# Performance work log

Hardware: AMD Instinct MI355X
Metric: run time of the kernel (lower is better)

Reference implementation:

```python
import jax, jax.numpy as jnp
import numpy as np

B, N, K = 2, 8192, 16
C_IN, C_OUT = 32, 64
EPS = 1e-6


def _bn(x, g, b, axes):
    m = jnp.mean(x, axes, keepdims=True)
    v = jnp.var(x, axes, keepdims=True)
    return (x - m) * jax.lax.rsqrt(v + EPS) * g + b


def _leaky(x, s):
    return jnp.where(x >= 0, x, s * x)


def _knn(coords, k):
    # brute-force euclidean KNN, self point included (dist 0)
    sq = jnp.sum(coords * coords, -1)  # (B,N)
    d2 = sq[:, :, None] + sq[:, None, :] - 2.0 * jnp.einsum('bnd,bmd->bnm', coords, coords)
    neg, idx = jax.lax.top_k(-d2, k)  # (B,N,K)
    dist = jnp.sqrt(jnp.clip(-neg, 1e-12, None))
    return idx, dist


def setup_inputs() -> dict:
    key = jax.random.key(0)
    ks = jax.random.split(key, 12)
    h = C_OUT // 2
    w = lambda k, s: jax.random.normal(k, s, jnp.float32) * 0.05
    return {
        'coords': jax.random.normal(ks[0], (B, N, 3), jnp.float32),
        'features': jax.random.normal(ks[1], (B, N, C_IN), jnp.float32),
        'W_mlp1': w(ks[2], (C_IN, h)), 'b_mlp1': jnp.zeros(h, jnp.float32),
        'W_lse1': w(ks[3], (10, h)), 'b_lse1': jnp.zeros(h, jnp.float32),
        'g_lse1': jnp.ones(h, jnp.float32), 'be_lse1': jnp.zeros(h, jnp.float32),
        'W_att1_lin': w(ks[4], (C_OUT, C_OUT)),
        'W_att1_mlp': w(ks[5], (C_OUT, h)), 'b_att1_mlp': jnp.zeros(h, jnp.float32),
        'g_att1': jnp.ones(h, jnp.float32), 'be_att1': jnp.zeros(h, jnp.float32),
        'W_lse2': w(ks[6], (10, h)), 'b_lse2': jnp.zeros(h, jnp.float32),
        'g_lse2': jnp.ones(h, jnp.float32), 'be_lse2': jnp.zeros(h, jnp.float32),
        'W_att2_lin': w(ks[7], (C_OUT, C_OUT)),
        'W_att2_mlp': w(ks[8], (C_OUT, C_OUT)), 'b_att2_mlp': jnp.zeros(C_OUT, jnp.float32),
        'g_att2': jnp.ones(C_OUT, jnp.float32), 'be_att2': jnp.zeros(C_OUT, jnp.float32),
        'W_mlp2': w(ks[9], (C_OUT, 2 * C_OUT)), 'b_mlp2': jnp.zeros(2 * C_OUT, jnp.float32),
        'W_short': w(ks[10], (C_IN, 2 * C_OUT)), 'b_short': jnp.zeros(2 * C_OUT, jnp.float32),
        'g_short': jnp.ones(2 * C_OUT, jnp.float32), 'be_short': jnp.zeros(2 * C_OUT, jnp.float32),
    }


def _forward(coords, features, W_mlp1, b_mlp1, W_lse1, b_lse1, g_lse1, be_lse1,
             W_att1_lin, W_att1_mlp, b_att1_mlp, g_att1, be_att1,
             W_lse2, b_lse2, g_lse2, be_lse2,
             W_att2_lin, W_att2_mlp, b_att2_mlp, g_att2, be_att2,
             W_mlp2, b_mlp2, W_short, b_short, g_short, be_short):
    idx, dist = _knn(coords, K)                     # (B,N,K)
    nbr = jax.vmap(lambda c, i: c[i])(coords, idx)  # gather neighbor coords (B,N,K,3)
    center = jnp.broadcast_to(coords[:, :, None, :], nbr.shape)
    # spatial encoding: [center, neighbor, center-neighbor, dist] -> 10 channels
    se = jnp.concatenate([center, nbr, center - nbr, dist[..., None]], -1)  # (B,N,K,10)

    # mlp1 (1x1 conv + LeakyReLU(0.2)), no BN
    x = _leaky(features @ W_mlp1 + b_mlp1, 0.2)     # (B,N,h)

    # LocSE 1: shared MLP (BN train-mode + ReLU) on spatial enc, concat features
    sp1 = jax.nn.relu(_bn(se @ W_lse1 + b_lse1, g_lse1, be_lse1, (0, 1, 2)))  # (B,N,K,h)
    x1 = jnp.concatenate([sp1, jnp.broadcast_to(x[:, :, None, :], sp1.shape)], -1)  # (B,N,K,2h)

    # attention pooling 1: softmax over neighbors K, weighted sum, MLP+BN+ReLU
    sc1 = jax.nn.softmax(x1 @ W_att1_lin, axis=2)
    p1 = jnp.sum(sc1 * x1, axis=2)                  # (B,N,2h)
    x = jax.nn.relu(_bn(p1 @ W_att1_mlp + b_att1_mlp, g_att1, be_att1, (0, 1)))  # (B,N,h)

    # LocSE 2 + attention pooling 2 (same KNN, separate weights)
    sp2 = jax.nn.relu(_bn(se @ W_lse2 + b_lse2, g_lse2, be_lse2, (0, 1, 2)))
    x2 = jnp.concatenate([sp2, jnp.broadcast_to(x[:, :, None, :], sp2.shape)], -1)
    sc2 = jax.nn.softmax(x2 @ W_att2_lin, axis=2)
    p2 = jnp.sum(sc2 * x2, axis=2)
    x = jax.nn.relu(_bn(p2 @ W_att2_mlp + b_att2_mlp, g_att2, be_att2, (0, 1)))  # (B,N,C_OUT)

    # mlp2 (no BN, no act) + shortcut (BN, no act), residual LeakyReLU(0.01)
    x = x @ W_mlp2 + b_mlp2                          # (B,N,2*C_OUT)
    short = _bn(features @ W_short + b_short, g_short, be_short, (0, 1))
    out = _leaky(x + short, 0.01)
    # match torch layout (B, 2*C_OUT, N, 1)
    return jnp.transpose(out, (0, 2, 1))[..., None]


def reference(coords, features, W_mlp1, b_mlp1, W_lse1, b_lse1, g_lse1, be_lse1,
              W_att1_lin, W_att1_mlp, b_att1_mlp, g_att1, be_att1,
              W_lse2, b_lse2, g_lse2, be_lse2,
              W_att2_lin, W_att2_mlp, b_att2_mlp, g_att2, be_att2,
              W_mlp2, b_mlp2, W_short, b_short, g_short, be_short):
    return _forward(coords, features, W_mlp1, b_mlp1, W_lse1, b_lse1, g_lse1, be_lse1,
                    W_att1_lin, W_att1_mlp, b_att1_mlp, g_att1, be_att1,
                    W_lse2, b_lse2, g_lse2, be_lse2,
                    W_att2_lin, W_att2_mlp, b_att2_mlp, g_att2, be_att2,
                    W_mlp2, b_mlp2, W_short, b_short, g_short, be_short)
```

## Files before the change

kernel.cpp:

```cpp
#include <hip/hip_runtime.h>
#include <cfloat>
#include <cmath>

#define DEV __device__ __forceinline__

constexpr int BB = 2, NN = 8192, KK = 16, CIN = 32, HH = 32, CO = 64, C2 = 128;
constexpr int BNTOT = BB * NN;
constexpr int BNKROWS = BB * NN * KK;
constexpr float EPSF = 1e-6f;

constexpr int S_LSE1 = 0, S_LSE2 = 64, S_ATT1 = 128, S_ATT2 = 192, S_SHORT = 320, S_TOTAL = 576;

constexpr size_t OFF_CP4   = 0;
constexpr size_t OFF_SE    = OFF_CP4 + (size_t)BNTOT * 4;
constexpr size_t OFF_XF    = OFF_SE + (size_t)BNKROWS * 10;
constexpr size_t OFF_SHORT = OFF_XF + (size_t)BNTOT * HH;
constexpr size_t OFF_PRE1  = OFF_SHORT + (size_t)BNTOT * C2;
constexpr size_t OFF_PRE2  = OFF_PRE1 + (size_t)BNTOT * HH;
constexpr size_t OFF_STATS = OFF_PRE2 + (size_t)BNTOT * CO;

__global__ __launch_bounds__(256) void k_prep(const float* __restrict__ coords,
                                              float4* __restrict__ cp4) {
#pragma clang fp contract(off)
    int i = blockIdx.x * 256 + threadIdx.x;
    if (i >= BNTOT) return;
    float x = coords[3 * i], y = coords[3 * i + 1], z = coords[3 * i + 2];
    float sq = (x * x + y * y) + z * z;
    cp4[i] = make_float4(x, y, z, sq);
}

DEV float dist2(float4 qc, float4 c) {
#pragma clang fp contract(off)
    float dot = (qc.x * c.x + qc.y * c.y) + qc.z * c.z;
    return (qc.w + c.w) - 2.0f * dot;
}

DEV unsigned encf(float f) {
    unsigned u = __float_as_uint(f);
    return (u & 0x80000000u) ? ~u : (u | 0x80000000u);
}
DEV float decf(unsigned e) {
    unsigned u = (e & 0x80000000u) ? (e & 0x7FFFFFFFu) : ~e;
    return __uint_as_float(u);
}

DEV void ins16(float (&dl)[16], int (&il)[16], float d, int id) {
    float dk = d; int jk = id;
#pragma unroll
    for (int r = 0; r < 16; ++r) {
        bool c = dk < dl[r];
        float td = dl[r]; int ti = il[r];
        dl[r] = c ? dk : dl[r]; il[r] = c ? jk : il[r];
        dk = c ? td : dk; jk = c ? ti : jk;
    }
}

DEV void ins16_lex(float (&dl)[16], int (&il)[16], float d, int id) {
    float dk = d; int jk = id;
#pragma unroll
    for (int r = 0; r < 16; ++r) {
        bool c = (dk < dl[r]) || (dk == dl[r] && jk < il[r]);
        float td = dl[r]; int ti = il[r];
        dl[r] = c ? dk : dl[r]; il[r] = c ? jk : il[r];
        dk = c ? td : dk; jk = c ? ti : jk;
    }
}

__global__ __launch_bounds__(256) void k_knn(const float4* __restrict__ cp4,
                                             float* __restrict__ se) {
    __shared__ float mdl[16][16][17];
    __shared__ int   mil[16][16][17];
    __shared__ unsigned thr[16];
    uint2 (*buf)[256] = reinterpret_cast<uint2(*)[256]>(&mdl[0][0][0]);

    int t = threadIdx.x;
    int b = blockIdx.x >> 9;
    int qbase = (blockIdx.x & 511) * 16;
    int ql = t & 15, part = t >> 4;
    const float4* cp = cp4 + (size_t)b * NN;
    float4 qc = cp[qbase + ql];

    if (t < 16) thr[t] = encf(FLT_MAX);
    __syncthreads();

    float dl[16]; int il[16];
#pragma unroll
    for (int i = 0; i < 16; ++i) { dl[i] = FLT_MAX; il[i] = 0; }

    int cb = part * 512;
#pragma unroll
    for (int k = 0; k < 16; ++k) ins16(dl, il, dist2(qc, cp[cb + k]), cb + k);
    atomicMin(&thr[ql], encf(dl[15]));
    float Tf = dl[15];
    int cnt = 0;

    float4 n0 = cp[cb + 16], n1 = cp[cb + 17], n2 = cp[cb + 18], n3 = cp[cb + 19];
    unsigned te = thr[ql];
    for (int j = cb + 16; j < cb + 512; j += 4) {
        float4 c0 = n0, c1 = n1, c2 = n2, c3 = n3;
        n0 = cp[j + 4]; n1 = cp[j + 5]; n2 = cp[j + 6]; n3 = cp[j + 7];
        float d0 = dist2(qc, c0), d1 = dist2(qc, c1), d2v = dist2(qc, c2), d3 = dist2(qc, c3);
        bool p0 = d0 <= Tf, p1 = d1 <= Tf, p2 = d2v <= Tf, p3 = d3 <= Tf;
        if (__any(p0 | p1 | p2 | p3)) {
            if (p0) { buf[cnt][t] = make_uint2(__float_as_uint(d0), (unsigned)(j)); ++cnt; }
            if (p1) { buf[cnt][t] = make_uint2(__float_as_uint(d1), (unsigned)(j + 1)); ++cnt; }
            if (p2) { buf[cnt][t] = make_uint2(__float_as_uint(d2v), (unsigned)(j + 2)); ++cnt; }
            if (p3) { buf[cnt][t] = make_uint2(__float_as_uint(d3), (unsigned)(j + 3)); ++cnt; }
            if (__any(cnt >= 4)) {
#pragma unroll
                for (int s = 0; s < 7; ++s) {
                    if (s < cnt) {
                        uint2 v = buf[s][t];
                        float d = __uint_as_float(v.x);
                        if (d < dl[15]) ins16(dl, il, d, (int)v.y);
                    }
                }
                cnt = 0;
                atomicMin(&thr[ql], encf(dl[15]));
            }
        }
        Tf = decf(te);
        te = thr[ql];
    }
    if (__any(cnt > 0)) {
#pragma unroll
        for (int s = 0; s < 7; ++s) {
            if (s < cnt) {
                uint2 v = buf[s][t];
                float d = __uint_as_float(v.x);
                if (d < dl[15]) ins16(dl, il, d, (int)v.y);
            }
        }
    }

    __syncthreads();
#pragma unroll
    for (int i = 0; i < 16; ++i) { mdl[part][ql][i] = dl[i]; mil[part][ql][i] = il[i]; }
    __syncthreads();

    for (int half = 8; half >= 1; half >>= 1) {
        if (part < half) {
#pragma unroll
            for (int i = 0; i < 16; ++i) {
                float d = mdl[part + half][ql][i]; int id = mil[part + half][ql][i];
                if (d < dl[15] || (d == dl[15] && id < il[15])) ins16_lex(dl, il, d, id);
            }
#pragma unroll
            for (int i = 0; i < 16; ++i) { mdl[part][ql][i] = dl[i]; mil[part][ql][i] = il[i]; }
        }
        __syncthreads();
    }

    {
        int qq = t >> 4, k = t & 15;
        float d2s = mdl[0][qq][k]; int id = mil[0][qq][k];
        float4 qc2 = cp[qbase + qq];
        float4 nb = cp[id];
        float dist = sqrtf(fmaxf(d2s, 1e-12f));
        float* sp = se + ((size_t)(b * NN + qbase + qq) * KK + k) * 10;
        sp[0] = qc2.x; sp[1] = qc2.y; sp[2] = qc2.z;
        sp[3] = nb.x;  sp[4] = nb.y;  sp[5] = nb.z;
        sp[6] = qc2.x - nb.x; sp[7] = qc2.y - nb.y; sp[8] = qc2.z - nb.z;
        sp[9] = dist;
    }
}

__global__ __launch_bounds__(128) void k_feat(const float* __restrict__ feat,
                                              const float* __restrict__ Wm1, const float* __restrict__ bm1,
                                              const float* __restrict__ Wsh, const float* __restrict__ bsh,
                                              float* __restrict__ xf, float* __restrict__ short_pre,
                                              double* __restrict__ stats) {
    __shared__ float fl[32][33];
    int t = threadIdx.x;
    int pbase = blockIdx.x * 32;
    float wcol[32];
#pragma unroll
    for (int i = 0; i < 32; ++i) wcol[i] = Wsh[i * C2 + t];
    float wm[32];
    if (t < 32) {
#pragma unroll
        for (int i = 0; i < 32; ++i) wm[i] = Wm1[i * HH + t];
    }
    float bs = bsh[t];
    float bm = (t < 32) ? bm1[t] : 0.f;
    double s = 0.0, s2 = 0.0;

    for (int e = t; e < 1024; e += 128) {
        int p = e >> 5, i = e & 31;
        fl[p][i] = feat[(size_t)(pbase + p) * CIN + i];
    }
    __syncthreads();
    for (int p = 0; p < 32; ++p) {
        float acc = bs;
#pragma unroll
        for (int i = 0; i < 32; ++i) acc += fl[p][i] * wcol[i];
        int gp = pbase + p;
        short_pre[(size_t)gp * C2 + t] = acc;
        s += acc; s2 += (double)acc * acc;
        if (t < 32) {
            float xv = bm;
#pragma unroll
            for (int i = 0; i < 32; ++i) xv += fl[p][i] * wm[i];
            xf[(size_t)gp * HH + t] = xv >= 0.f ? xv : 0.2f * xv;
        }
    }
    atomicAdd(&stats[S_SHORT + t], s);
    atomicAdd(&stats[S_SHORT + C2 + t], s2);
}

__global__ __launch_bounds__(256) void k_lse_stats(const float* __restrict__ se,
                                                   const float* __restrict__ W1, const float* __restrict__ b1,
                                                   const float* __restrict__ W2, const float* __restrict__ b2,
                                                   double* __restrict__ stats) {
    __shared__ float srows[256][10];
    __shared__ double red[4][64][2];
    int t = threadIdx.x;
    int c = t & 63, grp = t >> 6;
    int ch = c & 31; bool second = c >= 32;
    const float* W = second ? W2 : W1;
    float wcol[10];
#pragma unroll
    for (int d = 0; d < 10; ++d) wcol[d] = W[d * HH + ch];
    float bb = second ? b2[ch] : b1[ch];
    double s = 0.0, s2 = 0.0;
    int rbase = blockIdx.x * 512;

    for (int tile = 0; tile < 2; ++tile) {
        __syncthreads();
        const float* src = se + (size_t)(rbase + tile * 256) * 10;
        for (int e = t; e < 2560; e += 256) srows[e / 10][e % 10] = src[e];
        __syncthreads();
        int r0 = grp * 64;
        for (int r = r0; r < r0 + 64; ++r) {
            float acc = bb;
#pragma unroll
            for (int d = 0; d < 10; ++d) acc += srows[r][d] * wcol[d];
            s += acc; s2 += (double)acc * acc;
        }
    }
    red[grp][c][0] = s; red[grp][c][1] = s2;
    __syncthreads();
    if (grp == 0) {
        for (int g = 1; g < 4; ++g) { s += red[g][c][0]; s2 += red[g][c][1]; }
        int base = second ? S_LSE2 : S_LSE1;
        atomicAdd(&stats[base + ch], s);
        atomicAdd(&stats[base + 32 + ch], s2);
    }
}

DEV float2 fin_pair(const double* stats, int sbase, int ch, int nch, double M,
                    const float* g, const float* be) {
    double mean = stats[sbase + ch] / M;
    double var = stats[sbase + nch + ch] / M - mean * mean;
    double scd = (double)g[ch] / sqrt(var + (double)EPSF);
    return make_float2((float)scd, (float)((double)be[ch] - mean * scd));
}

template <int OUTC, bool SECOND>
__global__ __launch_bounds__(256) void k_att(const float* __restrict__ se,
                                             const float* __restrict__ featsrc,
                                             const float* __restrict__ Wlse, const float* __restrict__ blse,
                                             const float* __restrict__ Wlin,
                                             const float* __restrict__ Wmlp, const float* __restrict__ bmlp,
                                             double* __restrict__ stats, int lse_sbase, int feat_sbase, int stat_base,
                                             const float* __restrict__ g_lse, const float* __restrict__ be_lse,
                                             const float* __restrict__ g_f, const float* __restrict__ be_f,
                                             float* __restrict__ preout) {
    __shared__ __align__(16) float wlt[64][68];
    __shared__ float wm[64][OUTC];
    __shared__ __align__(16) float x1[4][16][40];
    __shared__ float fv[4][32];
    __shared__ float p1b[4][64];
    __shared__ double red[4][OUTC][2];

    int t = threadIdx.x, w = t >> 6, c = t & 63;
    int ch = c & 31, half = c >> 5;
    for (int e = t; e < 4096; e += 256) wlt[e & 63][e >> 6] = Wlin[e];
    for (int e = t; e < 64 * OUTC; e += 256) wm[e / OUTC][e % OUTC] = Wmlp[e];

    float wf[10]; float bf;
    {
        float2 p = fin_pair(stats, lse_sbase, ch, 32, (double)BNKROWS, g_lse, be_lse);
#pragma unroll
        for (int d = 0; d < 10; ++d) wf[d] = Wlse[d * 32 + ch] * p.x;
        bf = blse[ch] * p.x + p.y;
    }
    float fa = 1.f, fb = 0.f;
    if (SECOND && c >= 32) {
        float2 p = fin_pair(stats, feat_sbase, ch, 32, (double)BNTOT, g_f, be_f);
        fa = p.x; fb = p.y;
    }
    double s = 0.0, s2 = 0.0;
    __syncthreads();

    for (int i = 0; i < 4; ++i) {
        int p = blockIdx.x * 16 + w * 4 + i;

        int kbase = half * 8;
        const float* sp = se + (size_t)p * (KK * 10) + kbase * 10;
        float myv[8];
#pragma unroll
        for (int kk = 0; kk < 8; ++kk) {
            float acc = bf;
#pragma unroll
            for (int d = 0; d < 10; ++d) acc += sp[kk * 10 + d] * wf[d];
            myv[kk] = fmaxf(acc, 0.f);
        }
#pragma unroll
        for (int kk = 0; kk < 8; ++kk) x1[w][kbase + kk][ch] = myv[kk];

        float xv = 0.f;
        if (c >= 32) {
            xv = featsrc[(size_t)p * 32 + ch];
            if (SECOND) xv = fmaxf(xv * fa + fb, 0.f);
            fv[w][ch] = xv;
        }

        float col[16];
        if (c < 32) {
#pragma unroll
            for (int kk = 0; kk < 8; ++kk) col[kk] = myv[kk];
#pragma unroll
            for (int kk = 0; kk < 8; ++kk) col[8 + kk] = x1[w][8 + kk][ch];
        } else {
#pragma unroll
            for (int k = 0; k < 16; ++k) col[k] = xv;
        }

        float cst = 0.f;
#pragma unroll
        for (int dg = 8; dg < 16; ++dg) {
            float4 wv = *(const float4*)&wlt[c][dg * 4];
            float4 xvv = *(const float4*)&fv[w][(dg - 8) * 4];
            cst += xvv.x * wv.x + xvv.y * wv.y + xvv.z * wv.z + xvv.w * wv.w;
        }
        float scv[16];
#pragma unroll
        for (int k = 0; k < 16; ++k) scv[k] = cst;
        for (int dg = 0; dg < 8; ++dg) {
            float4 wv = *(const float4*)&wlt[c][dg * 4];
#pragma unroll
            for (int k = 0; k < 16; ++k) {
                float4 xvv = *(const float4*)&x1[w][k][dg * 4];
                scv[k] += xvv.x * wv.x + xvv.y * wv.y + xvv.z * wv.z + xvv.w * wv.w;
            }
        }
        float m = scv[0];
#pragma unroll
        for (int k = 1; k < 16; ++k) m = fmaxf(m, scv[k]);
        float sum = 0.f, p1 = 0.f;
#pragma unroll
        for (int k = 0; k < 16; ++k) { float e = __expf(scv[k] - m); sum += e; p1 += e * col[k]; }
        p1 /= sum;
        p1b[w][c] = p1;

        if (c < OUTC) {
            float acc = bmlp[c];
#pragma unroll
            for (int d = 0; d < 64; ++d) acc += p1b[w][d] * wm[d][c];
            preout[(size_t)p * OUTC + c] = acc;
            s += acc; s2 += (double)acc * acc;
        }
    }
    if (c < OUTC) { red[w][c][0] = s; red[w][c][1] = s2; }
    __syncthreads();
    if (t < OUTC) {
        double ts = red[0][t][0], ts2 = red[0][t][1];
        for (int g = 1; g < 4; ++g) { ts += red[g][t][0]; ts2 += red[g][t][1]; }
        atomicAdd(&stats[stat_base + t], ts);
        atomicAdd(&stats[stat_base + OUTC + t], ts2);
    }
}

__global__ __launch_bounds__(256) void k_out(const float* __restrict__ pre2,
                                             const float* __restrict__ short_pre,
                                             const float* __restrict__ W2, const float* __restrict__ b2,
                                             const double* __restrict__ stats,
                                             const float* __restrict__ g_a2, const float* __restrict__ be_a2,
                                             const float* __restrict__ g_s, const float* __restrict__ be_s,
                                             float* __restrict__ out) {
    __shared__ __align__(16) float w2[64][128];
    __shared__ float sc2[64], sh2[64], scs[128], shs[128], bb[128];
    int t = threadIdx.x;
    int pl = t & 31, seg = t >> 5;
    for (int e = t; e < 8192; e += 256) w2[e >> 7][e & 127] = W2[e];
    if (t < 64) { float2 p = fin_pair(stats, S_ATT2, t, 64, (double)BNTOT, g_a2, be_a2); sc2[t] = p.x; sh2[t] = p.y; }
    if (t >= 64 && t < 192) { int ch = t - 64; float2 p = fin_pair(stats, S_SHORT, ch, 128, (double)BNTOT, g_s, be_s); scs[ch] = p.x; shs[ch] = p.y; }
    if (t < 128) bb[t] = b2[t];
    __syncthreads();

    int p = blockIdx.x * 32 + pl;
    int b = p >> 13, n = p & 8191;
    const float* pr = pre2 + (size_t)p * 64;
    float xa[64];
#pragma unroll
    for (int c = 0; c < 64; c += 4) {
        float4 v = *(const float4*)&pr[c];
        xa[c + 0] = fmaxf(v.x * sc2[c + 0] + sh2[c + 0], 0.f);
        xa[c + 1] = fmaxf(v.y * sc2[c + 1] + sh2[c + 1], 0.f);
        xa[c + 2] = fmaxf(v.z * sc2[c + 2] + sh2[c + 2], 0.f);
        xa[c + 3] = fmaxf(v.w * sc2[c + 3] + sh2[c + 3], 0.f);
    }
    const float* shp = short_pre + (size_t)p * 128;
    int obase = seg * 16;
    for (int o = obase; o < obase + 16; o += 4) {
        float a0 = bb[o], a1 = bb[o + 1], a2 = bb[o + 2], a3 = bb[o + 3];
#pragma unroll
        for (int cc = 0; cc < 64; ++cc) {
            float4 wv = *(const float4*)&w2[cc][o];
            float x = xa[cc];
            a0 += x * wv.x; a1 += x * wv.y; a2 += x * wv.z; a3 += x * wv.w;
        }
        float4 sv = *(const float4*)&shp[o];
        float r0 = a0 + (sv.x * scs[o] + shs[o]);
        float r1 = a1 + (sv.y * scs[o + 1] + shs[o + 1]);
        float r2 = a2 + (sv.z * scs[o + 2] + shs[o + 2]);
        float r3 = a3 + (sv.w * scs[o + 3] + shs[o + 3]);
        out[((size_t)(b * C2 + o + 0)) * NN + n] = r0 >= 0.f ? r0 : 0.01f * r0;
        out[((size_t)(b * C2 + o + 1)) * NN + n] = r1 >= 0.f ? r1 : 0.01f * r1;
        out[((size_t)(b * C2 + o + 2)) * NN + n] = r2 >= 0.f ? r2 : 0.01f * r2;
        out[((size_t)(b * C2 + o + 3)) * NN + n] = r3 >= 0.f ? r3 : 0.01f * r3;
    }
}

extern "C" void kernel_launch(void* const* d_in, const int* in_sizes, int n_in,
                              void* d_out, int out_size, void* d_ws, size_t ws_size,
                              hipStream_t stream) {
    const float* coords    = (const float*)d_in[0];
    const float* features  = (const float*)d_in[1];
    const float* W_mlp1    = (const float*)d_in[2];
    const float* b_mlp1    = (const float*)d_in[3];
    const float* W_lse1    = (const float*)d_in[4];
    const float* b_lse1    = (const float*)d_in[5];
    const float* g_lse1    = (const float*)d_in[6];
    const float* be_lse1   = (const float*)d_in[7];
    const float* W_att1_lin= (const float*)d_in[8];
    const float* W_att1_mlp= (const float*)d_in[9];
    const float* b_att1_mlp= (const float*)d_in[10];
    const float* g_att1    = (const float*)d_in[11];
    const float* be_att1   = (const float*)d_in[12];
    const float* W_lse2    = (const float*)d_in[13];
    const float* b_lse2    = (const float*)d_in[14];
    const float* g_lse2    = (const float*)d_in[15];
    const float* be_lse2   = (const float*)d_in[16];
    const float* W_att2_lin= (const float*)d_in[17];
    const float* W_att2_mlp= (const float*)d_in[18];
    const float* b_att2_mlp= (const float*)d_in[19];
    const float* g_att2    = (const float*)d_in[20];
    const float* be_att2   = (const float*)d_in[21];
    const float* W_mlp2    = (const float*)d_in[22];
    const float* b_mlp2    = (const float*)d_in[23];
    const float* W_short   = (const float*)d_in[24];
    const float* b_short   = (const float*)d_in[25];
    const float* g_short   = (const float*)d_in[26];
    const float* be_short  = (const float*)d_in[27];

    float* ws = (float*)d_ws;
    float4* cp4      = (float4*)(ws + OFF_CP4);
    float* se        = ws + OFF_SE;
    float* xf        = ws + OFF_XF;
    float* short_pre = ws + OFF_SHORT;
    float* pre1      = ws + OFF_PRE1;
    float* pre2      = ws + OFF_PRE2;
    double* stats    = (double*)(ws + OFF_STATS);
    float* out       = (float*)d_out;

    hipMemsetAsync(stats, 0, S_TOTAL * sizeof(double), stream);

    k_prep<<<BNTOT / 256, 256, 0, stream>>>(coords, cp4);
    k_knn<<<1024, 256, 0, stream>>>(cp4, se);
    k_feat<<<512, 128, 0, stream>>>(features, W_mlp1, b_mlp1, W_short, b_short,
                                    xf, short_pre, stats);
    k_lse_stats<<<512, 256, 0, stream>>>(se, W_lse1, b_lse1, W_lse2, b_lse2, stats);
    k_att<32, false><<<1024, 256, 0, stream>>>(se, xf, W_lse1, b_lse1, W_att1_lin,
                                               W_att1_mlp, b_att1_mlp, stats,
                                               S_LSE1, 0, S_ATT1,
                                               g_lse1, be_lse1, nullptr, nullptr, pre1);
    k_att<64, true><<<1024, 256, 0, stream>>>(se, pre1, W_lse2, b_lse2, W_att2_lin,
                                              W_att2_mlp, b_att2_mlp, stats,
                                              S_LSE2, S_ATT1, S_ATT2,
                                              g_lse2, be_lse2, g_att1, be_att1, pre2);
    k_out<<<BNTOT / 32, 256, 0, stream>>>(pre2, short_pre, W_mlp2, b_mlp2, stats,
                                          g_att2, be_att2, g_short, be_short, out);
}
```

Baseline: 420.0 us.

## Seed KNN thresholds via Morton-sorted neighborhood prepass, then single-pass filtered scan

Adds a Morton-code bucketing of points (count, scan, scatter) and a seed kernel that computes an upper bound on each query's 16th-nearest distance from 256 nearby points in sorted order. The main KNN kernel then filters all candidates against this fixed bound, collects survivors into shared memory, and does a single sort per query. If a query has too many survivors it falls back to a wave-wide brute-force pass. This removes the per-thread insertion lists, atomic threshold sharing and the tree merge, at the cost of four extra small kernels and a serial per-query survivor sort.

```diff
diff --git a/kernel.cpp b/kernel.cpp
--- a/kernel.cpp
+++ b/kernel.cpp
@@ -8,6 +8,8 @@
 constexpr int BNTOT = BB * NN;
 constexpr int BNKROWS = BB * NN * KK;
 constexpr float EPSF = 1e-6f;
+constexpr int NCELL = 4096;
+constexpr int CAP = 128;
 
 constexpr int S_LSE1 = 0, S_LSE2 = 64, S_ATT1 = 128, S_ATT2 = 192, S_SHORT = 320, S_TOTAL = 576;
 
@@ -18,15 +20,68 @@
 constexpr size_t OFF_PRE1  = OFF_SHORT + (size_t)BNTOT * C2;
 constexpr size_t OFF_PRE2  = OFF_PRE1 + (size_t)BNTOT * HH;
 constexpr size_t OFF_STATS = OFF_PRE2 + (size_t)BNTOT * CO;
+constexpr size_t OFF_COUNTS= OFF_STATS + 2 * S_TOTAL;
+constexpr size_t OFF_TB    = OFF_COUNTS + 2 * NCELL;
+constexpr size_t OFF_CODE  = OFF_SHORT;
+constexpr size_t OFF_CPS   = OFF_CODE + 16384;
+constexpr size_t OFF_OIDX  = OFF_CPS + (size_t)BNTOT * 4 + 16;
+
+DEV unsigned spr3(unsigned v) {
+    return (v & 1u) | ((v & 2u) << 2) | ((v & 4u) << 4) | ((v & 8u) << 6);
+}
 
 __global__ __launch_bounds__(256) void k_prep(const float* __restrict__ coords,
-                                              float4* __restrict__ cp4) {
+                                              float4* __restrict__ cp4,
+                                              int* __restrict__ code, int* __restrict__ counts) {
 #pragma clang fp contract(off)
     int i = blockIdx.x * 256 + threadIdx.x;
     if (i >= BNTOT) return;
     float x = coords[3 * i], y = coords[3 * i + 1], z = coords[3 * i + 2];
     float sq = (x * x + y * y) + z * z;
     cp4[i] = make_float4(x, y, z, sq);
+    const float inv = 16.f / 8.8f;
+    int ix = min(15, max(0, (int)floorf((x + 4.4f) * inv)));
+    int iy = min(15, max(0, (int)floorf((y + 4.4f) * inv)));
+    int iz = min(15, max(0, (int)floorf((z + 4.4f) * inv)));
+    unsigned m = spr3(ix) | (spr3(iy) << 1) | (spr3(iz) << 2);
+    code[i] = (int)m;
+    atomicAdd(&counts[((i >> 13) << 12) + m], 1);
+}
+
+__global__ __launch_bounds__(256) void k_scan(int* __restrict__ counts) {
+    __shared__ int lds[256];
+    int t = threadIdx.x;
+    for (int b = 0; b < 2; ++b) {
+        int base = b * NCELL;
+        int v[16]; int s = 0;
+#pragma unroll
+        for (int k = 0; k < 16; ++k) { int tmp = counts[base + t * 16 + k]; v[k] = s; s += tmp; }
+        lds[t] = s;
+        __syncthreads();
+        for (int o = 1; o < 256; o <<= 1) {
+            int u = (t >= o) ? lds[t - o] : 0;
+            __syncthreads();
+            lds[t] += u;
+            __syncthreads();
+        }
+        int off = lds[t] - s;
+#pragma unroll
+        for (int k = 0; k < 16; ++k) counts[base + t * 16 + k] = off + v[k];
+        __syncthreads();
+    }
+}
+
+__global__ __launch_bounds__(256) void k_scatter(const float4* __restrict__ cp4,
+                                                 const int* __restrict__ code,
+                                                 int* __restrict__ cursor,
+                                                 float4* __restrict__ cps, int* __restrict__ oidx) {
+    int i = blockIdx.x * 256 + threadIdx.x;
+    if (i >= BNTOT) return;
+    int b = i >> 13, n = i & 8191;
+    int c = code[i];
+    int pos = atomicAdd(&cursor[(b << 12) + c], 1);
+    cps[(b << 13) + pos] = cp4[i];
+    oidx[(b << 13) + pos] = n;
 }
 
 DEV float dist2(float4 qc, float4 c) {
@@ -35,23 +90,14 @@
     return (qc.w + c.w) - 2.0f * dot;
 }
 
-DEV unsigned encf(float f) {
-    unsigned u = __float_as_uint(f);
-    return (u & 0x80000000u) ? ~u : (u | 0x80000000u);
-}
-DEV float decf(unsigned e) {
-    unsigned u = (e & 0x80000000u) ? (e & 0x7FFFFFFFu) : ~e;
-    return __uint_as_float(u);
-}
-
-DEV void ins16(float (&dl)[16], int (&il)[16], float d, int id) {
-    float dk = d; int jk = id;
+DEV void insv16(float (&dl)[16], float d) {
+    float dk = d;
 #pragma unroll
     for (int r = 0; r < 16; ++r) {
         bool c = dk < dl[r];
-        float td = dl[r]; int ti = il[r];
-        dl[r] = c ? dk : dl[r]; il[r] = c ? jk : il[r];
-        dk = c ? td : dk; jk = c ? ti : jk;
+        float td = dl[r];
+        dl[r] = c ? dk : dl[r];
+        dk = c ? td : dk;
     }
 }
 
@@ -66,94 +112,111 @@
     }
 }
 
+__global__ __launch_bounds__(256) void k_seed(const float4* __restrict__ cps,
+                                              const int* __restrict__ oidx,
+                                              float* __restrict__ tbound) {
+    int g = blockIdx.x * 256 + threadIdx.x;
+    int b = g >> 13, p = g & 8191;
+    const float4* cb_ = cps + ((size_t)b << 13);
+    float4 qc = cb_[p];
+    int s = p - 128;
+    s = s < 0 ? 0 : (s > NN - 256 ? NN - 256 : s);
+    float dl[16];
+#pragma unroll
+    for (int i = 0; i < 16; ++i) dl[i] = FLT_MAX;
+    for (int j = 0; j < 256; j += 4) {
+        float4 c0 = cb_[s + j], c1 = cb_[s + j + 1], c2 = cb_[s + j + 2], c3 = cb_[s + j + 3];
+        float d0 = dist2(qc, c0), d1 = dist2(qc, c1), d2v = dist2(qc, c2), d3 = dist2(qc, c3);
+        if (d0 < dl[15]) insv16(dl, d0);
+        if (d1 < dl[15]) insv16(dl, d1);
+        if (d2v < dl[15]) insv16(dl, d2v);
+        if (d3 < dl[15]) insv16(dl, d3);
+    }
+    tbound[(b << 13) + oidx[(b << 13) + p]] = dl[15];
+}
+
 __global__ __launch_bounds__(256) void k_knn(const float4* __restrict__ cp4,
+                                             const float* __restrict__ tbound,
                                              float* __restrict__ se) {
-    __shared__ float mdl[16][16][17];
-    __shared__ int   mil[16][16][17];
-    __shared__ unsigned thr[16];
-    uint2 (*buf)[256] = reinterpret_cast<uint2(*)[256]>(&mdl[0][0][0]);
+    __shared__ uint2 surv[16][CAP + 1];
+    __shared__ int scnt[16];
+    __shared__ float sd[16][17];
+    __shared__ int   si[16][17];
 
     int t = threadIdx.x;
     int b = blockIdx.x >> 9;
     int qbase = (blockIdx.x & 511) * 16;
     int ql = t & 15, part = t >> 4;
-    const float4* cp = cp4 + (size_t)b * NN;
-    float4 qc = cp[qbase + ql];
-
-    if (t < 16) thr[t] = encf(FLT_MAX);
-    __syncthreads();
-
-    float dl[16]; int il[16];
-#pragma unroll
-    for (int i = 0; i < 16; ++i) { dl[i] = FLT_MAX; il[i] = 0; }
+    int wv = t >> 6, lane = t & 63;
+    const float4* cp = cp4 + ((size_t)b << 13);
+    int q = qbase + ql;
+    float4 qc = cp[q];
+    float T = tbound[(b << 13) + q];
+
+    if (t < 16) scnt[t] = 0;
+    __syncthreads();
 
     int cb = part * 512;
-#pragma unroll
-    for (int k = 0; k < 16; ++k) ins16(dl, il, dist2(qc, cp[cb + k]), cb + k);
-    atomicMin(&thr[ql], encf(dl[15]));
-    float Tf = dl[15];
-    int cnt = 0;
-
-    float4 n0 = cp[cb + 16], n1 = cp[cb + 17], n2 = cp[cb + 18], n3 = cp[cb + 19];
-    unsigned te = thr[ql];
-    for (int j = cb + 16; j < cb + 512; j += 4) {
+    float4 n0 = cp[cb], n1 = cp[cb + 1], n2 = cp[cb + 2], n3 = cp[cb + 3];
+    for (int j = cb; j < cb + 512; j += 4) {
         float4 c0 = n0, c1 = n1, c2 = n2, c3 = n3;
         n0 = cp[j + 4]; n1 = cp[j + 5]; n2 = cp[j + 6]; n3 = cp[j + 7];
         float d0 = dist2(qc, c0), d1 = dist2(qc, c1), d2v = dist2(qc, c2), d3 = dist2(qc, c3);
-        bool p0 = d0 <= Tf, p1 = d1 <= Tf, p2 = d2v <= Tf, p3 = d3 <= Tf;
+        bool p0 = d0 <= T, p1 = d1 <= T, p2 = d2v <= T, p3 = d3 <= T;
         if (__any(p0 | p1 | p2 | p3)) {
-            if (p0) { buf[cnt][t] = make_uint2(__float_as_uint(d0), (unsigned)(j)); ++cnt; }
-            if (p1) { buf[cnt][t] = make_uint2(__float_as_uint(d1), (unsigned)(j + 1)); ++cnt; }
-            if (p2) { buf[cnt][t] = make_uint2(__float_as_uint(d2v), (unsigned)(j + 2)); ++cnt; }
-            if (p3) { buf[cnt][t] = make_uint2(__float_as_uint(d3), (unsigned)(j + 3)); ++cnt; }
-            if (__any(cnt >= 4)) {
-#pragma unroll
-                for (int s = 0; s < 7; ++s) {
-                    if (s < cnt) {
-                        uint2 v = buf[s][t];
-                        float d = __uint_as_float(v.x);
-                        if (d < dl[15]) ins16(dl, il, d, (int)v.y);
-                    }
+            if (p0) { int pos = atomicAdd(&scnt[ql], 1); if (pos < CAP) surv[ql][pos] = make_uint2(__float_as_uint(d0), (unsigned)j); }
+            if (p1) { int pos = atomicAdd(&scnt[ql], 1); if (pos < CAP) surv[ql][pos] = make_uint2(__float_as_uint(d1), (unsigned)(j + 1)); }
+            if (p2) { int pos = atomicAdd(&scnt[ql], 1); if (pos < CAP) surv[ql][pos] = make_uint2(__float_as_uint(d2v), (unsigned)(j + 2)); }
+            if (p3) { int pos = atomicAdd(&scnt[ql], 1); if (pos < CAP) surv[ql][pos] = make_uint2(__float_as_uint(d3), (unsigned)(j + 3)); }
+        }
+    }
+    __syncthreads();
+
+    for (int q2 = wv; q2 < 16; q2 += 4) {
+        if (scnt[q2] > CAP) {
+            float4 qc2 = cp[qbase + q2];
+            float dl[16]; int il[16];
+#pragma unroll
+            for (int i = 0; i < 16; ++i) { dl[i] = FLT_MAX; il[i] = 0x7fffffff; }
+            for (int i = 0; i < 128; ++i) {
+                int j = lane + (i << 6);
+                float d = dist2(qc2, cp[j]);
+                if (d < dl[15] || (d == dl[15] && j < il[15])) ins16_lex(dl, il, d, j);
+            }
+            for (int o = 1; o < 64; o <<= 1) {
+                float dd[16]; int ii[16];
+#pragma unroll
+                for (int i = 0; i < 16; ++i) { dd[i] = __shfl_xor(dl[i], o); ii[i] = __shfl_xor(il[i], o); }
+#pragma unroll
+                for (int i = 0; i < 16; ++i) {
+                    if (dd[i] < dl[15] || (dd[i] == dl[15] && ii[i] < il[15])) ins16_lex(dl, il, dd[i], ii[i]);
                 }
-                cnt = 0;
-                atomicMin(&thr[ql], encf(dl[15]));
             }
-        }
-        Tf = decf(te);
-        te = thr[ql];
-    }
-    if (__any(cnt > 0)) {
-#pragma unroll
-        for (int s = 0; s < 7; ++s) {
-            if (s < cnt) {
-                uint2 v = buf[s][t];
-                float d = __uint_as_float(v.x);
-                if (d < dl[15]) ins16(dl, il, d, (int)v.y);
+            if (lane == 0) {
+#pragma unroll
+                for (int i = 0; i < 16; ++i) { sd[q2][i] = dl[i]; si[q2][i] = il[i]; }
             }
         }
     }
 
-    __syncthreads();
-#pragma unroll
-    for (int i = 0; i < 16; ++i) { mdl[part][ql][i] = dl[i]; mil[part][ql][i] = il[i]; }
-    __syncthreads();
-
-    for (int half = 8; half >= 1; half >>= 1) {
-        if (part < half) {
-#pragma unroll
-            for (int i = 0; i < 16; ++i) {
-                float d = mdl[part + half][ql][i]; int id = mil[part + half][ql][i];
-                if (d < dl[15] || (d == dl[15] && id < il[15])) ins16_lex(dl, il, d, id);
-            }
-#pragma unroll
-            for (int i = 0; i < 16; ++i) { mdl[part][ql][i] = dl[i]; mil[part][ql][i] = il[i]; }
-        }
-        __syncthreads();
-    }
+    if (t < 16 && scnt[t] <= CAP) {
+        int n = scnt[t];
+        float dl[16]; int il[16];
+#pragma unroll
+        for (int i = 0; i < 16; ++i) { dl[i] = FLT_MAX; il[i] = 0x7fffffff; }
+        for (int s2 = 0; s2 < n; ++s2) {
+            uint2 v = surv[t][s2];
+            float d = __uint_as_float(v.x); int id = (int)v.y;
+            if (d < dl[15] || (d == dl[15] && id < il[15])) ins16_lex(dl, il, d, id);
+        }
+#pragma unroll
+        for (int i = 0; i < 16; ++i) { sd[t][i] = dl[i]; si[t][i] = il[i]; }
+    }
+    __syncthreads();
 
     {
         int qq = t >> 4, k = t & 15;
-        float d2s = mdl[0][qq][k]; int id = mil[0][qq][k];
+        float d2s = sd[qq][k]; int id = si[qq][k];
         float4 qc2 = cp[qbase + qq];
         float4 nb = cp[id];
         float dist = sqrtf(fmaxf(d2s, 1e-12f));
@@ -463,12 +526,20 @@
     float* pre1      = ws + OFF_PRE1;
     float* pre2      = ws + OFF_PRE2;
     double* stats    = (double*)(ws + OFF_STATS);
+    int* counts      = (int*)(ws + OFF_COUNTS);
+    float* tbound    = ws + OFF_TB;
+    int* code        = (int*)(ws + OFF_CODE);
+    float4* cps      = (float4*)(ws + OFF_CPS);
+    int* oidxArr     = (int*)(ws + OFF_OIDX);
     float* out       = (float*)d_out;
 
-    hipMemsetAsync(stats, 0, S_TOTAL * sizeof(double), stream);
-
-    k_prep<<<BNTOT / 256, 256, 0, stream>>>(coords, cp4);
-    k_knn<<<1024, 256, 0, stream>>>(cp4, se);
+    hipMemsetAsync(stats, 0, S_TOTAL * 8 + 2 * NCELL * 4, stream);
+
+    k_prep<<<BNTOT / 256, 256, 0, stream>>>(coords, cp4, code, counts);
+    k_scan<<<1, 256, 0, stream>>>(counts);
+    k_scatter<<<BNTOT / 256, 256, 0, stream>>>(cp4, code, counts, cps, oidxArr);
+    k_seed<<<BNTOT / 256, 256, 0, stream>>>(cps, oidxArr, tbound);
+    k_knn<<<1024, 256, 0, stream>>>(cp4, tbound, se);
     k_feat<<<512, 128, 0, stream>>>(features, W_mlp1, b_mlp1, W_short, b_short,
                                     xf, short_pre, stats);
     k_lse_stats<<<512, 256, 0, stream>>>(se, W_lse1, b_lse1, W_lse2, b_lse2, stats);
```

Measured after the change: 606.0 us. 44.3% more time.
